# Kernel optimization log

Hardware: AMD Instinct MI355X
Metric: run time of the kernel (lower is better)

The kernel has to match this reference:

```python
import jax, jax.numpy as jnp
import numpy as np

WEIGHT = 1.0  # init kwarg: loss weight
N = 4096
D_FEAT = 128


def _pairwise_dist(x):
    # x: [n, d] -> D: [n, n] Euclidean distances (safe sqrt for grad at 0)
    sq = jnp.sum(x * x, axis=-1)
    d2 = sq[:, None] + sq[None, :] - 2.0 * (x @ x.T)
    d2 = jnp.maximum(d2, 0.0)
    pos = d2 > 1e-12
    return jnp.where(pos, jnp.sqrt(jnp.where(pos, d2, 1.0)), 0.0)


def _prim_mst(D):
    # Vectorized Prim: returns (parents, children) of the n-1 MST edges.
    # filtration value (VR complex truncated at max_dimension=1).
    n = D.shape[0]
    INF = jnp.finfo(D.dtype).max
    visited0 = jnp.zeros(n, dtype=bool).at[0].set(True)
    mind0 = D[0]
    parent0 = jnp.zeros(n, dtype=jnp.int32)

    def step(carry, _):
        visited, mind, parent = carry
        j = jnp.argmin(jnp.where(visited, INF, mind))
        pj = parent[j]
        visited = visited.at[j].set(True)
        better = (D[j] < mind) & (~visited)
        mind = jnp.where(better, D[j], mind)
        parent = jnp.where(better, j, parent)
        return (visited, mind, parent), (pj, j.astype(jnp.int32))

    _, (pjs, js) = jax.lax.scan(step, (visited0, mind0, parent0), None, length=n - 1)
    return pjs, js


def _h1_persistence(x):
    # H1 diagram for VR complex with max_dimension=1: a 1-cycle is born when a
    # non-MST edge appears; with no 2-simplices it never dies, so deaths are
    # capped at the maximal filtration value. Persistence = cap - birth.
    n = x.shape[0]
    D = _pairwise_dist(x)
    pjs, js = _prim_mst(D)
    tree = jnp.zeros((n, n), dtype=bool)
    tree = tree.at[pjs, js].set(True)
    tree = tree | tree.T
    iu = np.triu_indices(n, 1)  # static indices
    births = D[iu]              # [n*(n-1)/2]
    is_tree = tree[iu]
    cap = jnp.max(D)
    # tree edges are H0 (not H1): give them zero persistence (diagonal points)
    return jnp.where(is_tree, 0.0, cap - births)


def _wasserstein_1d(p1, p2):
    # 1-Wasserstein between equal-size persistence multisets via sorted matching
    # (deaths share a common cap per diagram, so matching by sorted persistence).
    return jnp.sum(jnp.abs(jnp.sort(p1) - jnp.sort(p2)))


def setup_inputs() -> dict:
    key = jax.random.key(0)
    k1, k2, k3, k4 = jax.random.split(key, 4)
    return {
        "graph1_features": jax.random.normal(k1, (N, D_FEAT), dtype=jnp.float32),
        "graph1_edges": jax.random.randint(k2, (2, 8 * N), 0, N, dtype=jnp.int64),
        "graph2_features": jax.random.normal(k3, (N, D_FEAT), dtype=jnp.float32),
        "graph2_edges": jax.random.randint(k4, (2, 8 * N), 0, N, dtype=jnp.int64),
    }


def reference(graph1_features, graph1_edges, graph2_features, graph2_edges):
    # edge tensors are unused: the torch forward builds VR complexes from the
    # point clouds only (build_from_points), matching the original module.
    p1 = _h1_persistence(graph1_features)
    p2 = _h1_persistence(graph2_features)
    return WEIGHT * _wasserstein_1d(p1, p2)
```

## Files before the change

### kernel.cpp

```cpp
#include <hip/hip_runtime.h>
#include <stdint.h>

#define NN 4096
#define DF 128
#define NBINS 16384
#define NSLAB 256
#define BORUVKA_ROUNDS 12

typedef __attribute__((ext_vector_type(8))) short short8;
typedef __attribute__((ext_vector_type(4))) float floatx4;
typedef __attribute__((ext_vector_type(4))) unsigned short ushort4_t;
typedef __attribute__((ext_vector_type(8))) unsigned short ushort8_t;
typedef __attribute__((ext_vector_type(4))) int int4_t;
typedef __attribute__((ext_vector_type(2))) unsigned uvec2;
typedef __attribute__((ext_vector_type(2))) int ivec2;

__device__ __forceinline__ unsigned bin_of(float v, float scale) {
  if (v < 0.f) v = 0.f;
  unsigned b = (unsigned)(v * scale);
  return b >= (unsigned)NBINS ? (unsigned)(NBINS - 1) : b;
}

__device__ __forceinline__ void gload16(const unsigned short* g, unsigned short* l) {
  __builtin_amdgcn_global_load_lds(
      (const __attribute__((address_space(1))) void*)g,
      (__attribute__((address_space(3))) void*)l, 16, 0, 0);
}

__global__ void k_rownorm(const float* __restrict__ x1, const float* __restrict__ x2,
                          float* __restrict__ sq) {
  int i = blockIdx.x * blockDim.x + threadIdx.x;
  if (i >= 2 * NN) return;
  const float* x = (i < NN) ? x1 : x2;
  int r = i & (NN - 1);
  const float* row = x + (size_t)r * DF;
  float s = 0.f;
  for (int k = 0; k < DF; ++k) s += row[k] * row[k];
  sq[i] = s;
}

__global__ __launch_bounds__(256) void k_bound(const float* __restrict__ sq,
                                               float* __restrict__ hdrf) {
  int t = threadIdx.x;
  float m = 0.f;
  for (int i = t; i < 2 * NN; i += 256) m = fmaxf(m, sq[i]);
  for (int off = 32; off > 0; off >>= 1) m = fmaxf(m, __shfl_down(m, off, 64));
  __shared__ float wm[4];
  if ((t & 63) == 0) wm[t >> 6] = m;
  __syncthreads();
  if (t == 0) {
    float mm = fmaxf(fmaxf(wm[0], wm[1]), fmaxf(wm[2], wm[3]));
    float dbound = 2.f * sqrtf(mm);
    hdrf[2] = 65535.f / dbound;
    hdrf[3] = dbound / 65535.f;
  }
}

__global__ void k_split(const float* __restrict__ x1, const float* __restrict__ x2,
                        unsigned short* __restrict__ xh, unsigned short* __restrict__ xl) {
  int i = blockIdx.x * blockDim.x + threadIdx.x;
  if (i >= 2 * NN * DF) return;
  const float* x = (i < NN * DF) ? x1 : x2;
  float v = x[i & (NN * DF - 1)];
  unsigned u = __float_as_uint(v);
  unsigned hu = u & 0xffff0000u;
  float hf = __uint_as_float(hu);
  float lf = v - hf;
  unsigned lu = __float_as_uint(lf) & 0xffff0000u;
  xh[i] = (unsigned short)(hu >> 16);
  xl[i] = (unsigned short)(lu >> 16);
}

__global__ void k_binit(int* __restrict__ comp, unsigned long long* __restrict__ compbest,
                        int* __restrict__ mstcnt, int* __restrict__ ncomp) {
  int i = blockIdx.x * blockDim.x + threadIdx.x;
  if (i >= 2 * NN) return;
  comp[i] = i & (NN - 1);
  compbest[i] = ~0ull;
  if ((i & (NN - 1)) == 0) {
    mstcnt[i >> 12] = 0;
    ncomp[i >> 12] = NN;
  }
}

#define SJ 136
__global__ __launch_bounds__(256) void k_dist(const unsigned short* __restrict__ Xhi,
                                              const unsigned short* __restrict__ Xlo,
                                              const float* __restrict__ sq,
                                              const float* __restrict__ hdrf,
                                              unsigned short* __restrict__ Qbase,
                                              unsigned* __restrict__ segmin_base,
                                              unsigned* __restrict__ caps) {
  int bi = blockIdx.y, bj = blockIdx.x;
  if (bi > bj) return;
  bool offdiag = (bi != bj);
  int g = blockIdx.z;
  const unsigned short* xh = Xhi + (size_t)g * NN * DF;
  const unsigned short* xl = Xlo + (size_t)g * NN * DF;
  const float* sqg = sq + g * NN;
  unsigned short* Q = Qbase + (size_t)g * NN * NN;
  unsigned* smg = segmin_base + (size_t)g * NN * 32;
  float qs = hdrf[2];
  int t = threadIdx.x;
  int w = t >> 6, lane = t & 63;
  int m = lane & 15, quad = lane >> 4;
  int iw = (w >> 1) * 64, jw = (w & 1) * 64;
  int i0 = bi * 128 + iw;
  int j0 = bj * 128 + jw;

  __shared__ __align__(16) unsigned short SB[128 * SJ];

  int baseRow = (w < 2) ? bi * 128 : bj * 128;
  const unsigned short* src = (w == 0 || w == 2) ? xh : xl;
  unsigned short* ldsPiece = &SB[w * 4096];
  int rsub = lane >> 2;
  int kpart = (lane & 3) ^ ((lane >> 3) & 3);
  int fr = (quad ^ ((m >> 1) & 3)) << 3;

  floatx4 acc[4][4];
#pragma unroll
  for (int ti = 0; ti < 4; ++ti)
#pragma unroll
    for (int tj = 0; tj < 4; ++tj) acc[ti][tj] = (floatx4){0.f, 0.f, 0.f, 0.f};

  for (int s = 0; s < 4; ++s) {
    int kc = s * 32;
    if (s) __syncthreads();
#pragma unroll
    for (int i = 0; i < 8; ++i) {
      const unsigned short* gp =
          src + (size_t)(baseRow + i * 16 + rsub) * DF + kc + kpart * 8;
      gload16(gp, &ldsPiece[i * 512]);
    }
    __syncthreads();
    short8 ah[4], al[4], bh[4], bl[4];
#pragma unroll
    for (int ti = 0; ti < 4; ++ti) {
      int ra = (iw + ti * 16 + m) * 32 + fr;
      int rb = (jw + ti * 16 + m) * 32 + fr;
      ah[ti] = *(const short8*)&SB[ra];
      al[ti] = *(const short8*)&SB[4096 + ra];
      bh[ti] = *(const short8*)&SB[8192 + rb];
      bl[ti] = *(const short8*)&SB[12288 + rb];
    }
#pragma unroll
    for (int ti = 0; ti < 4; ++ti)
#pragma unroll
      for (int tj = 0; tj < 4; ++tj) {
        acc[ti][tj] = __builtin_amdgcn_mfma_f32_16x16x32_bf16(ah[ti], bh[tj], acc[ti][tj], 0, 0, 0);
        acc[ti][tj] = __builtin_amdgcn_mfma_f32_16x16x32_bf16(ah[ti], bl[tj], acc[ti][tj], 0, 0, 0);
        acc[ti][tj] = __builtin_amdgcn_mfma_f32_16x16x32_bf16(al[ti], bh[tj], acc[ti][tj], 0, 0, 0);
      }
  }

  float sqj[4];
#pragma unroll
  for (int tj = 0; tj < 4; ++tj) sqj[tj] = sqg[j0 + tj * 16 + m];
  float mx = 0.f;
  ushort4_t qv[4][4];
#pragma unroll
  for (int ti = 0; ti < 4; ++ti) {
    int ib = i0 + ti * 16 + quad * 4;
    float sqiv[4];
#pragma unroll
    for (int r = 0; r < 4; ++r) sqiv[r] = sqg[ib + r];
#pragma unroll
    for (int tj = 0; tj < 4; ++tj) {
#pragma unroll
      for (int r = 0; r < 4; ++r) {
        float d2 = sqiv[r] + sqj[tj] - 2.f * acc[ti][tj][r];
        d2 = fmaxf(d2, 0.f);
        float d = (d2 > 1e-12f) ? sqrtf(d2) : 0.f;
        mx = fmaxf(mx, d);
        unsigned q = (unsigned)(d * qs + 0.5f);
        if (q > 65535u) q = 65535u;
        qv[ti][tj][r] = (unsigned short)q;
      }
    }
  }

  __syncthreads();
  unsigned short* T = SB;
  int sub = t >> 4, l16 = t & 15;
  int l31 = lane & 31, half = lane >> 5;

  auto prefill_rows = [&](int rbase, int cbase, int segidx, bool exdiag) {
#pragma unroll 4
    for (int ii = 0; ii < 16; ++ii) {
      int rr = w * 32 + ii * 2 + half;
      uvec2 vv = *(const uvec2*)&T[rr * SJ + l31 * 4];
      int row = rbase + rr;
      unsigned qq[4] = {vv[0] & 0xffffu, vv[0] >> 16, vv[1] & 0xffffu, vv[1] >> 16};
      unsigned kmin = 0xffffffffu;
#pragma unroll
      for (int u = 0; u < 4; ++u) {
        int cl = l31 * 4 + u;
        if (!exdiag || (cbase + cl) != row) {
          unsigned key = (qq[u] << 7) | (unsigned)cl;
          if (key < kmin) kmin = key;
        }
      }
#pragma unroll
      for (int off2 = 1; off2 < 32; off2 <<= 1) {
        unsigned o = (unsigned)__shfl_xor((int)kmin, off2, 32);
        if (o < kmin) kmin = o;
      }
      if (l31 == 0) smg[(size_t)row * 32 + segidx] = kmin;
    }
  };

#pragma unroll
  for (int ti = 0; ti < 4; ++ti) {
    int il = iw + ti * 16 + quad * 4;
#pragma unroll
    for (int tj = 0; tj < 4; ++tj) {
      int jl = jw + tj * 16 + m;
      *(ushort4_t*)&T[jl * SJ + il] = qv[ti][tj];
    }
  }
  __syncthreads();
#pragma unroll
  for (int k = 0; k < 8; ++k) {
    int jl = k * 16 + sub;
    int4_t v = *(const int4_t*)&T[jl * SJ + l16 * 8];
    *(int4_t*)&Q[(size_t)(bj * 128 + jl) * NN + bi * 128 + l16 * 8] = v;
  }
  prefill_rows(bj * 128, bi * 128, bi, !offdiag);

  if (offdiag) {
    __syncthreads();
#pragma unroll
    for (int ti = 0; ti < 4; ++ti) {
      int il = iw + ti * 16 + quad * 4;
#pragma unroll
      for (int tj = 0; tj < 4; ++tj) {
        int jl = jw + tj * 16 + m;
#pragma unroll
        for (int r = 0; r < 4; ++r) T[(il + r) * SJ + jl] = qv[ti][tj][r];
      }
    }
    __syncthreads();
#pragma unroll
    for (int k = 0; k < 8; ++k) {
      int il = k * 16 + sub;
      int4_t v = *(const int4_t*)&T[il * SJ + l16 * 8];
      *(int4_t*)&Q[(size_t)(bi * 128 + il) * NN + bj * 128 + l16 * 8] = v;
    }
    prefill_rows(bi * 128, bj * 128, bj, false);
  }

  for (int off = 32; off > 0; off >>= 1) mx = fmaxf(mx, __shfl_down(mx, off, 64));
  __shared__ float wmax[4];
  if (lane == 0) wmax[w] = mx;
  __syncthreads();
  if (t == 0) {
    float mm = fmaxf(fmaxf(wmax[0], wmax[1]), fmaxf(wmax[2], wmax[3]));
    atomicMax(&caps[g], __float_as_uint(mm));
  }
}

__global__ __launch_bounds__(256) void k_minedge(const unsigned short* __restrict__ Qbase,
                                                 const unsigned* __restrict__ segmin_base,
                                                 const int* __restrict__ comp_base,
                                                 unsigned long long* __restrict__ compbest_base,
                                                 const int* __restrict__ ncomp) {
  int g = blockIdx.y;
  if (ncomp[g] == 1) return;
  int w = threadIdx.x >> 6, lane = threadIdx.x & 63;
  int v = blockIdx.x * 4 + w;
  const int* comp = comp_base + g * NN;
  unsigned long long* cbest = compbest_base + (size_t)g * NN;
  int cv = comp[v];
  const unsigned* sm = segmin_base + ((size_t)g * NN + (size_t)v) * 32;

  unsigned key28 = 0xffffffffu;
  bool incomp = false;
  if (lane < 32) {
    unsigned k23 = sm[lane];
    unsigned q = k23 >> 7, cl = k23 & 127u;
    unsigned col = (unsigned)lane * 128u + cl;
    key28 = (q << 12) | col;
    incomp = (comp[col] == cv);
  }
  unsigned a = (lane < 32 && !incomp) ? key28 : 0xffffffffu;
#pragma unroll
  for (int off = 1; off < 64; off <<= 1) {
    unsigned o = (unsigned)__shfl_xor((int)a, off, 64);
    if (o < a) a = o;
  }
  unsigned best = a;

  unsigned long long flags = __ballot(lane < 32 && incomp && key28 < best);
  if (flags) {
    const unsigned short* row = Qbase + ((size_t)g * NN + (size_t)v) * NN;
    while (flags) {
      int s = (int)(__ffsll((long long)flags) - 1);
      flags &= flags - 1;
      int j = s * 128 + (lane << 1);
      unsigned pq = *(const unsigned*)&row[j];
      ivec2 cj = *(const ivec2*)&comp[j];
      unsigned k1 = (cj[0] != cv) ? ((pq & 0xffffu) << 12) | (unsigned)j : 0xffffffffu;
      unsigned k2 = (cj[1] != cv) ? ((pq >> 16) << 12) | (unsigned)(j + 1) : 0xffffffffu;
      unsigned kk = k1 < k2 ? k1 : k2;
#pragma unroll
      for (int off = 1; off < 64; off <<= 1) {
        unsigned o = (unsigned)__shfl_xor((int)kk, off, 64);
        if (o < kk) kk = o;
      }
      if (kk < best) best = kk;
    }
  }
  if (lane == 0 && best != 0xffffffffu) {
    unsigned long long b64 = ((unsigned long long)(best >> 12) << 24) |
                             ((unsigned long long)v << 12) | (best & 0xfffu);
    atomicMin(&cbest[cv], b64);
  }
}

__global__ __launch_bounds__(1024) void k_hook(unsigned long long* __restrict__ compbest_base,
                                               int* __restrict__ comp_base,
                                               const float* __restrict__ hdrf,
                                               float* __restrict__ mstw_base,
                                               int* __restrict__ mstcnt,
                                               int* __restrict__ ncomp) {
  int g = blockIdx.x;
  if (ncomp[g] == 1) return;
  unsigned long long* cb = compbest_base + (size_t)g * NN;
  int* comp = comp_base + g * NN;
  float* mstw = mstw_base + g * (NN - 1);
  float qinv = hdrf[3];
  __shared__ int par[NN];
  __shared__ unsigned char live[NN];
  __shared__ int newcnt;
  int t = threadIdx.x;
  if (t == 0) newcnt = 0;
  for (int c = t; c < NN; c += 1024) {
    unsigned long long key = cb[c];
    bool a = (key != ~0ull);
    live[c] = a ? 1 : 0;
    int p = c;
    if (a) {
      int j = (int)(key & 0xfffull);
      p = comp[j];
    }
    par[c] = p;
  }
  __syncthreads();
  for (int c = t; c < NN; c += 1024) {
    int p = par[c];
    if (p != c && par[p] == c && c < p) par[c] = c;
  }
  __syncthreads();
  for (int c = t; c < NN; c += 1024) {
    if (live[c] && par[c] != c) {
      float w = (float)((unsigned)(cb[c] >> 24)) * qinv;
      int slot = atomicAdd(&mstcnt[g], 1);
      mstw[slot] = w;
    }
  }
  __syncthreads();
  for (;;) {
    int np[NN / 1024];
    bool ch = false;
    int k = 0;
    for (int c = t; c < NN; c += 1024, ++k) {
      int p = par[c];
      int pp = par[p];
      np[k] = pp;
      if (pp != p) ch = true;
    }
    __syncthreads();
    k = 0;
    for (int c = t; c < NN; c += 1024, ++k) par[c] = np[k];
    if (!__syncthreads_or(ch)) break;
  }
  int cnt = 0;
  for (int c = t; c < NN; c += 1024)
    if (live[c] && par[c] == c) cnt++;
  for (int off = 32; off > 0; off >>= 1) cnt += __shfl_down(cnt, off, 64);
  if ((t & 63) == 0 && cnt) atomicAdd(&newcnt, cnt);
  for (int v = t; v < NN; v += 1024) comp[v] = par[comp[v]];
  for (int c = t; c < NN; c += 1024) cb[c] = ~0ull;
  __syncthreads();
  if (t == 0) ncomp[g] = newcnt;
}

__global__ __launch_bounds__(256) void k_hist(const unsigned short* __restrict__ Qbase,
                                              const unsigned* __restrict__ caps,
                                              const float* __restrict__ hdrf,
                                              unsigned* __restrict__ Hs) {
  __shared__ unsigned h[NBINS];
  int t = threadIdx.x;
  for (int i = t; i < NBINS; i += 256) h[i] = 0;
  int b = blockIdx.x;
  int g = b >> 8, s = b & (NSLAB - 1);
  const unsigned short* Q = Qbase + (size_t)g * NN * NN;
  float cap = __uint_as_float(caps[g]);
  float capmax = fmaxf(__uint_as_float(caps[0]), __uint_as_float(caps[1]));
  float scale = (float)NBINS / capmax;
  float qinv = hdrf[3];
  __syncthreads();
  for (int p = s; p < NN / 2; p += NSLAB) {
#pragma unroll
    for (int half = 0; half < 2; ++half) {
      int rrow = half ? (NN - 1 - p) : p;
      const unsigned short* row = Q + (size_t)rrow * NN;
      int j0 = rrow + 1;
      int ja = (j0 + 7) & ~7;
      if (t < ja - j0)
        atomicAdd(&h[bin_of(cap - (float)row[j0 + t] * qinv, scale)], 1u);
      int nch = (NN - ja) >> 3;
      for (int c = t; c < nch; c += 256) {
        ushort8_t v8 = *(const ushort8_t*)&row[ja + c * 8];
#pragma unroll
        for (int u = 0; u < 8; ++u)
          atomicAdd(&h[bin_of(cap - (float)v8[u] * qinv, scale)], 1u);
      }
    }
  }
  __syncthreads();
  unsigned* slab = Hs + (size_t)b * NBINS;
  for (int i = t; i < NBINS; i += 256) slab[i] = h[i];
}

__global__ void k_treefix(const float* __restrict__ twbase, const unsigned* __restrict__ caps,
                          unsigned* __restrict__ Hs) {
  int g = blockIdx.y;
  unsigned* hist = Hs + (size_t)(g * NSLAB) * NBINS;
  float cap = __uint_as_float(caps[g]);
  float capmax = fmaxf(__uint_as_float(caps[0]), __uint_as_float(caps[1]));
  float scale = (float)NBINS / capmax;
  int idx = blockIdx.x * blockDim.x + threadIdx.x;
  if (idx < NN - 1) {
    float w = twbase[g * (NN - 1) + idx];
    atomicSub(&hist[bin_of(cap - w, scale)], 1u);
    atomicAdd(&hist[0], 1u);
  }
}

__global__ __launch_bounds__(256) void k_merge(const unsigned* __restrict__ Hs,
                                               unsigned* __restrict__ Hm) {
  int id = blockIdx.x * 256 + threadIdx.x;
  int g = id >> 14;
  int i = id & (NBINS - 1);
  const unsigned* base = Hs + (size_t)(g * NSLAB) * NBINS + i;
  unsigned sum = 0;
  for (int s = 0; s < NSLAB; ++s) sum += base[(size_t)s * NBINS];
  Hm[id] = sum;
}

__global__ __launch_bounds__(256) void k_w1(const unsigned* __restrict__ Hm,
                                            const unsigned* __restrict__ caps,
                                            float* __restrict__ out) {
  int t = threadIdx.x;
  const int PB = NBINS / 256;
  int base = t * PB;
  long long tsum = 0;
  for (int i = 0; i < PB; ++i)
    tsum += (long long)(int)(Hm[base + i] - Hm[NBINS + base + i]);
  int lane = t & 63, wid = t >> 6;
  long long incl = tsum;
  for (int off = 1; off < 64; off <<= 1) {
    long long o = __shfl_up(incl, off, 64);
    if (lane >= off) incl += o;
  }
  __shared__ long long wtot[4];
  if (lane == 63) wtot[wid] = incl;
  __syncthreads();
  long long run = incl - tsum;
  for (int w = 0; w < wid; ++w) run += wtot[w];
  unsigned long long local = 0;
  for (int i = 0; i < PB; ++i) {
    run += (long long)(int)(Hm[base + i] - Hm[NBINS + base + i]);
    local += (unsigned long long)(run < 0 ? -run : run);
  }
  for (int off = 32; off > 0; off >>= 1) local += __shfl_down(local, off, 64);
  __shared__ unsigned long long wl[4];
  if (lane == 0) wl[wid] = local;
  __syncthreads();
  if (t == 0) {
    float capmax = fmaxf(__uint_as_float(caps[0]), __uint_as_float(caps[1]));
    double dt = (double)capmax / (double)NBINS;
    out[0] = (float)((double)(wl[0] + wl[1] + wl[2] + wl[3]) * dt);
  }
}

__global__ void k_fail(float* out) { out[0] = -1234567.0f; }

extern "C" void kernel_launch(void* const* d_in, const int* in_sizes, int n_in,
                              void* d_out, int out_size, void* d_ws, size_t ws_size,
                              hipStream_t stream) {
  const float* x1 = (const float*)d_in[0];
  const float* x2 = (const float*)d_in[2];
  float* out = (float*)d_out;
  char* ws = (char*)d_ws;

  const size_t offQ = 0;
  const size_t offS = 2ull * NN * NN * 2ull;
  const size_t offHm = offS + 2ull * NSLAB * NBINS * 4ull;
  const size_t offHdr = offHm + 2ull * NBINS * 4ull;
  const size_t offSq = offHdr + 64;
  const size_t offTw = offSq + 2ull * NN * 4ull;
  const size_t offCb = (offTw + 2ull * (NN - 1) * 4ull + 7ull) & ~7ull;
  const size_t offSeg = offCb + 2ull * NN * 8ull;
  const size_t offCp = offSeg + 2ull * NN * 32ull * 4ull;
  const size_t offMeta = offCp + 2ull * NN * 4ull;
  const size_t needed = offMeta + 64;
  if (ws_size < needed) {
    hipLaunchKernelGGL(k_fail, dim3(1), dim3(1), 0, stream, out);
    return;
  }

  unsigned short* Qbase = (unsigned short*)(ws + offQ);
  unsigned* Hs = (unsigned*)(ws + offS);
  unsigned short* Xhi = (unsigned short*)(ws + offS);
  unsigned short* Xlo = (unsigned short*)(ws + offS + 2ull * NN * DF * 2ull);
  unsigned* Hm = (unsigned*)(ws + offHm);
  unsigned* caps = (unsigned*)(ws + offHdr);
  float* hdrf = (float*)(ws + offHdr);
  float* sq = (float*)(ws + offSq);
  float* tw = (float*)(ws + offTw);
  unsigned long long* compbest = (unsigned long long*)(ws + offCb);
  unsigned* segmin = (unsigned*)(ws + offSeg);
  int* comp = (int*)(ws + offCp);
  int* mstcnt = (int*)(ws + offMeta);
  int* ncomp = (int*)(ws + offMeta + 8);

  hipMemsetAsync(ws + offHdr, 0, 64, stream);

  hipLaunchKernelGGL(k_rownorm, dim3((2 * NN + 255) / 256), dim3(256), 0, stream, x1, x2, sq);
  hipLaunchKernelGGL(k_bound, dim3(1), dim3(256), 0, stream, sq, hdrf);
  hipLaunchKernelGGL(k_split, dim3((2 * NN * DF + 255) / 256), dim3(256), 0, stream,
                     x1, x2, Xhi, Xlo);
  hipLaunchKernelGGL(k_binit, dim3((2 * NN + 255) / 256), dim3(256), 0, stream,
                     comp, compbest, mstcnt, ncomp);
  hipLaunchKernelGGL(k_dist, dim3(NN / 128, NN / 128, 2), dim3(256), 0, stream,
                     Xhi, Xlo, sq, hdrf, Qbase, segmin, caps);
  for (int r = 0; r < BORUVKA_ROUNDS; ++r) {
    hipLaunchKernelGGL(k_minedge, dim3(NN / 4, 2), dim3(256), 0, stream,
                       Qbase, segmin, comp, compbest, ncomp);
    hipLaunchKernelGGL(k_hook, dim3(2), dim3(1024), 0, stream,
                       compbest, comp, hdrf, tw, mstcnt, ncomp);
  }
  hipLaunchKernelGGL(k_hist, dim3(2 * NSLAB), dim3(256), 0, stream, Qbase, caps, hdrf, Hs);
  hipLaunchKernelGGL(k_treefix, dim3(16, 2), dim3(256), 0, stream, tw, caps, Hs);
  hipLaunchKernelGGL(k_merge, dim3(2 * NBINS / 256), dim3(256), 0, stream, Hs, Hm);
  hipLaunchKernelGGL(k_w1, dim3(1), dim3(256), 0, stream, Hm, caps, out);
}
```

Baseline: 349.5 us.

## Fuse Boruvka min-edge and hook kernels with last-block-done pattern

Merges the per-round min-edge search and the component hooking step into one kernel. The last block to finish, detected through an atomic counter per graph, performs the hooking and pointer-jumping. This halves the number of launches across the Boruvka rounds. Blocks grow to 1024 threads with a 20KB shared-memory footprint. That may lower occupancy for the min-edge part and puts the serial hook step at the tail of the grid.

```diff
diff --git a/kernel.cpp b/kernel.cpp
--- a/kernel.cpp
+++ b/kernel.cpp
@@ -72,14 +72,17 @@
 }
 
 __global__ void k_binit(int* __restrict__ comp, unsigned long long* __restrict__ compbest,
-                        int* __restrict__ mstcnt, int* __restrict__ ncomp) {
+                        int* __restrict__ mstcnt, int* __restrict__ ncomp,
+                        int* __restrict__ done) {
   int i = blockIdx.x * blockDim.x + threadIdx.x;
   if (i >= 2 * NN) return;
   comp[i] = i & (NN - 1);
   compbest[i] = ~0ull;
   if ((i & (NN - 1)) == 0) {
-    mstcnt[i >> 12] = 0;
-    ncomp[i >> 12] = NN;
+    int g = i >> 12;
+    mstcnt[g] = 0;
+    ncomp[g] = NN;
+    done[g] = 0;
   }
 }
 
@@ -259,90 +262,92 @@
   }
 }
 
-__global__ __launch_bounds__(256) void k_minedge(const unsigned short* __restrict__ Qbase,
-                                                 const unsigned* __restrict__ segmin_base,
-                                                 const int* __restrict__ comp_base,
-                                                 unsigned long long* __restrict__ compbest_base,
-                                                 const int* __restrict__ ncomp) {
+__global__ __launch_bounds__(1024) void k_round(
+    const unsigned short* __restrict__ Qbase,
+    const unsigned* __restrict__ segmin_base,
+    int* __restrict__ comp_base,
+    unsigned long long* __restrict__ compbest_base,
+    const float* __restrict__ hdrf,
+    float* __restrict__ mstw_base,
+    int* __restrict__ mstcnt,
+    int* __restrict__ ncomp,
+    int* __restrict__ done) {
   int g = blockIdx.y;
   if (ncomp[g] == 1) return;
-  int w = threadIdx.x >> 6, lane = threadIdx.x & 63;
-  int v = blockIdx.x * 4 + w;
-  const int* comp = comp_base + g * NN;
+  int t = threadIdx.x;
+  int w = t >> 6, lane = t & 63;
+  int v = blockIdx.x * 16 + w;
+  int* comp = comp_base + g * NN;
   unsigned long long* cbest = compbest_base + (size_t)g * NN;
-  int cv = comp[v];
-  const unsigned* sm = segmin_base + ((size_t)g * NN + (size_t)v) * 32;
-
-  unsigned key28 = 0xffffffffu;
-  bool incomp = false;
-  if (lane < 32) {
-    unsigned k23 = sm[lane];
-    unsigned q = k23 >> 7, cl = k23 & 127u;
-    unsigned col = (unsigned)lane * 128u + cl;
-    key28 = (q << 12) | col;
-    incomp = (comp[col] == cv);
-  }
-  unsigned a = (lane < 32 && !incomp) ? key28 : 0xffffffffu;
-#pragma unroll
-  for (int off = 1; off < 64; off <<= 1) {
-    unsigned o = (unsigned)__shfl_xor((int)a, off, 64);
-    if (o < a) a = o;
-  }
-  unsigned best = a;
-
-  unsigned long long flags = __ballot(lane < 32 && incomp && key28 < best);
-  if (flags) {
-    const unsigned short* row = Qbase + ((size_t)g * NN + (size_t)v) * NN;
-    while (flags) {
-      int s = (int)(__ffsll((long long)flags) - 1);
-      flags &= flags - 1;
-      int j = s * 128 + (lane << 1);
-      unsigned pq = *(const unsigned*)&row[j];
-      ivec2 cj = *(const ivec2*)&comp[j];
-      unsigned k1 = (cj[0] != cv) ? ((pq & 0xffffu) << 12) | (unsigned)j : 0xffffffffu;
-      unsigned k2 = (cj[1] != cv) ? ((pq >> 16) << 12) | (unsigned)(j + 1) : 0xffffffffu;
-      unsigned kk = k1 < k2 ? k1 : k2;
-#pragma unroll
-      for (int off = 1; off < 64; off <<= 1) {
-        unsigned o = (unsigned)__shfl_xor((int)kk, off, 64);
-        if (o < kk) kk = o;
-      }
-      if (kk < best) best = kk;
-    }
-  }
-  if (lane == 0 && best != 0xffffffffu) {
-    unsigned long long b64 = ((unsigned long long)(best >> 12) << 24) |
-                             ((unsigned long long)v << 12) | (best & 0xfffu);
-    atomicMin(&cbest[cv], b64);
-  }
-}
-
-__global__ __launch_bounds__(1024) void k_hook(unsigned long long* __restrict__ compbest_base,
-                                               int* __restrict__ comp_base,
-                                               const float* __restrict__ hdrf,
-                                               float* __restrict__ mstw_base,
-                                               int* __restrict__ mstcnt,
-                                               int* __restrict__ ncomp) {
-  int g = blockIdx.x;
-  if (ncomp[g] == 1) return;
-  unsigned long long* cb = compbest_base + (size_t)g * NN;
-  int* comp = comp_base + g * NN;
+
+  {
+    int cv = comp[v];
+    const unsigned* sm = segmin_base + ((size_t)g * NN + (size_t)v) * 32;
+    unsigned key28 = 0xffffffffu;
+    bool incomp = false;
+    if (lane < 32) {
+      unsigned k23 = sm[lane];
+      unsigned q = k23 >> 7, cl = k23 & 127u;
+      unsigned col = (unsigned)lane * 128u + cl;
+      key28 = (q << 12) | col;
+      incomp = (comp[col] == cv);
+    }
+    unsigned a = (lane < 32 && !incomp) ? key28 : 0xffffffffu;
+#pragma unroll
+    for (int off = 1; off < 64; off <<= 1) {
+      unsigned o = (unsigned)__shfl_xor((int)a, off, 64);
+      if (o < a) a = o;
+    }
+    unsigned best = a;
+
+    unsigned long long flags = __ballot(lane < 32 && incomp && key28 < best);
+    if (flags) {
+      const unsigned short* row = Qbase + ((size_t)g * NN + (size_t)v) * NN;
+      while (flags) {
+        int s = (int)(__ffsll((long long)flags) - 1);
+        flags &= flags - 1;
+        int j = s * 128 + (lane << 1);
+        unsigned pq = *(const unsigned*)&row[j];
+        ivec2 cj = *(const ivec2*)&comp[j];
+        unsigned k1 = (cj[0] != cv) ? ((pq & 0xffffu) << 12) | (unsigned)j : 0xffffffffu;
+        unsigned k2 = (cj[1] != cv) ? ((pq >> 16) << 12) | (unsigned)(j + 1) : 0xffffffffu;
+        unsigned kk = k1 < k2 ? k1 : k2;
+#pragma unroll
+        for (int off = 1; off < 64; off <<= 1) {
+          unsigned o = (unsigned)__shfl_xor((int)kk, off, 64);
+          if (o < kk) kk = o;
+        }
+        if (kk < best) best = kk;
+      }
+    }
+    if (lane == 0 && best != 0xffffffffu) {
+      unsigned long long b64 = ((unsigned long long)(best >> 12) << 24) |
+                               ((unsigned long long)v << 12) | (best & 0xfffu);
+      atomicMin(&cbest[cv], b64);
+    }
+  }
+
+  __threadfence();
+  __syncthreads();
+  __shared__ int amlast;
+  if (t == 0) amlast = (atomicAdd(&done[g], 1) == (int)gridDim.x - 1) ? 1 : 0;
+  __syncthreads();
+  if (!amlast) return;
+
+  float qinv = hdrf[3];
+  unsigned long long* cb = cbest;
   float* mstw = mstw_base + g * (NN - 1);
-  float qinv = hdrf[3];
   __shared__ int par[NN];
   __shared__ unsigned char live[NN];
   __shared__ int newcnt;
-  int t = threadIdx.x;
   if (t == 0) newcnt = 0;
   for (int c = t; c < NN; c += 1024) {
-    unsigned long long key = cb[c];
+    unsigned long long key =
+        __hip_atomic_load(&cb[c], __ATOMIC_RELAXED, __HIP_MEMORY_SCOPE_AGENT);
     bool a = (key != ~0ull);
     live[c] = a ? 1 : 0;
     int p = c;
-    if (a) {
-      int j = (int)(key & 0xfffull);
-      p = comp[j];
-    }
+    if (a) p = comp[(int)(key & 0xfffull)];
     par[c] = p;
   }
   __syncthreads();
@@ -353,9 +358,11 @@
   __syncthreads();
   for (int c = t; c < NN; c += 1024) {
     if (live[c] && par[c] != c) {
-      float w = (float)((unsigned)(cb[c] >> 24)) * qinv;
+      unsigned long long key =
+          __hip_atomic_load(&cb[c], __ATOMIC_RELAXED, __HIP_MEMORY_SCOPE_AGENT);
+      float wgt = (float)((unsigned)(key >> 24)) * qinv;
       int slot = atomicAdd(&mstcnt[g], 1);
-      mstw[slot] = w;
+      mstw[slot] = wgt;
     }
   }
   __syncthreads();
@@ -379,10 +386,13 @@
     if (live[c] && par[c] == c) cnt++;
   for (int off = 32; off > 0; off >>= 1) cnt += __shfl_down(cnt, off, 64);
   if ((t & 63) == 0 && cnt) atomicAdd(&newcnt, cnt);
-  for (int v = t; v < NN; v += 1024) comp[v] = par[comp[v]];
+  for (int u = t; u < NN; u += 1024) comp[u] = par[comp[u]];
   for (int c = t; c < NN; c += 1024) cb[c] = ~0ull;
   __syncthreads();
-  if (t == 0) ncomp[g] = newcnt;
+  if (t == 0) {
+    ncomp[g] = newcnt;
+    done[g] = 0;
+  }
 }
 
 __global__ __launch_bounds__(256) void k_hist(const unsigned short* __restrict__ Qbase,
@@ -525,6 +535,7 @@
   int* comp = (int*)(ws + offCp);
   int* mstcnt = (int*)(ws + offMeta);
   int* ncomp = (int*)(ws + offMeta + 8);
+  int* done = (int*)(ws + offMeta + 16);
 
   hipMemsetAsync(ws + offHdr, 0, 64, stream);
 
@@ -533,14 +544,12 @@
   hipLaunchKernelGGL(k_split, dim3((2 * NN * DF + 255) / 256), dim3(256), 0, stream,
                      x1, x2, Xhi, Xlo);
   hipLaunchKernelGGL(k_binit, dim3((2 * NN + 255) / 256), dim3(256), 0, stream,
-                     comp, compbest, mstcnt, ncomp);
+                     comp, compbest, mstcnt, ncomp, done);
   hipLaunchKernelGGL(k_dist, dim3(NN / 128, NN / 128, 2), dim3(256), 0, stream,
                      Xhi, Xlo, sq, hdrf, Qbase, segmin, caps);
   for (int r = 0; r < BORUVKA_ROUNDS; ++r) {
-    hipLaunchKernelGGL(k_minedge, dim3(NN / 4, 2), dim3(256), 0, stream,
-                       Qbase, segmin, comp, compbest, ncomp);
-    hipLaunchKernelGGL(k_hook, dim3(2), dim3(1024), 0, stream,
-                       compbest, comp, hdrf, tw, mstcnt, ncomp);
+    hipLaunchKernelGGL(k_round, dim3(NN / 16, 2), dim3(1024), 0, stream,
+                       Qbase, segmin, comp, compbest, hdrf, tw, mstcnt, ncomp, done);
   }
   hipLaunchKernelGGL(k_hist, dim3(2 * NSLAB), dim3(256), 0, stream, Qbase, caps, hdrf, Hs);
   hipLaunchKernelGGL(k_treefix, dim3(16, 2), dim3(256), 0, stream, tw, caps, Hs);
```

Result: slower. 708.2 us (+102.7%).

## Move per-row segment-min computation from distance kernel into histogram pass

Applied to the files above, without the earlier changes.

The per-row 128-column segment minima used by the Boruvka min-edge search are no longer computed in the distance kernel. The histogram kernel, which now runs before the Boruvka rounds, computes them while it reads Q. The histogram pass now reads full rows rather than only the upper triangle. This is meant to lighten the distance kernel's epilogue and reuse the Q read the histogram pass already does, at the cost of roughly doubling the histogram kernel's global reads.

```diff
diff --git a/kernel.cpp b/kernel.cpp
--- a/kernel.cpp
+++ b/kernel.cpp
@@ -12,7 +12,6 @@
 typedef __attribute__((ext_vector_type(4))) unsigned short ushort4_t;
 typedef __attribute__((ext_vector_type(8))) unsigned short ushort8_t;
 typedef __attribute__((ext_vector_type(4))) int int4_t;
-typedef __attribute__((ext_vector_type(2))) unsigned uvec2;
 typedef __attribute__((ext_vector_type(2))) int ivec2;
 
 __device__ __forceinline__ unsigned bin_of(float v, float scale) {
@@ -89,7 +88,6 @@
                                               const float* __restrict__ sq,
                                               const float* __restrict__ hdrf,
                                               unsigned short* __restrict__ Qbase,
-                                              unsigned* __restrict__ segmin_base,
                                               unsigned* __restrict__ caps) {
   int bi = blockIdx.y, bj = blockIdx.x;
   if (bi > bj) return;
@@ -99,7 +97,6 @@
   const unsigned short* xl = Xlo + (size_t)g * NN * DF;
   const float* sqg = sq + g * NN;
   unsigned short* Q = Qbase + (size_t)g * NN * NN;
-  unsigned* smg = segmin_base + (size_t)g * NN * 32;
   float qs = hdrf[2];
   int t = threadIdx.x;
   int w = t >> 6, lane = t & 63;
@@ -182,32 +179,6 @@
   __syncthreads();
   unsigned short* T = SB;
   int sub = t >> 4, l16 = t & 15;
-  int l31 = lane & 31, half = lane >> 5;
-
-  auto prefill_rows = [&](int rbase, int cbase, int segidx, bool exdiag) {
-#pragma unroll 4
-    for (int ii = 0; ii < 16; ++ii) {
-      int rr = w * 32 + ii * 2 + half;
-      uvec2 vv = *(const uvec2*)&T[rr * SJ + l31 * 4];
-      int row = rbase + rr;
-      unsigned qq[4] = {vv[0] & 0xffffu, vv[0] >> 16, vv[1] & 0xffffu, vv[1] >> 16};
-      unsigned kmin = 0xffffffffu;
-#pragma unroll
-      for (int u = 0; u < 4; ++u) {
-        int cl = l31 * 4 + u;
-        if (!exdiag || (cbase + cl) != row) {
-          unsigned key = (qq[u] << 7) | (unsigned)cl;
-          if (key < kmin) kmin = key;
-        }
-      }
-#pragma unroll
-      for (int off2 = 1; off2 < 32; off2 <<= 1) {
-        unsigned o = (unsigned)__shfl_xor((int)kmin, off2, 32);
-        if (o < kmin) kmin = o;
-      }
-      if (l31 == 0) smg[(size_t)row * 32 + segidx] = kmin;
-    }
-  };
 
 #pragma unroll
   for (int ti = 0; ti < 4; ++ti) {
@@ -225,7 +196,6 @@
     int4_t v = *(const int4_t*)&T[jl * SJ + l16 * 8];
     *(int4_t*)&Q[(size_t)(bj * 128 + jl) * NN + bi * 128 + l16 * 8] = v;
   }
-  prefill_rows(bj * 128, bi * 128, bi, !offdiag);
 
   if (offdiag) {
     __syncthreads();
@@ -246,7 +216,6 @@
       int4_t v = *(const int4_t*)&T[il * SJ + l16 * 8];
       *(int4_t*)&Q[(size_t)(bi * 128 + il) * NN + bj * 128 + l16 * 8] = v;
     }
-    prefill_rows(bi * 128, bj * 128, bj, false);
   }
 
   for (int off = 32; off > 0; off >>= 1) mx = fmaxf(mx, __shfl_down(mx, off, 64));
@@ -257,6 +226,57 @@
     float mm = fmaxf(fmaxf(wmax[0], wmax[1]), fmaxf(wmax[2], wmax[3]));
     atomicMax(&caps[g], __float_as_uint(mm));
   }
+}
+
+__global__ __launch_bounds__(256) void k_hist(const unsigned short* __restrict__ Qbase,
+                                              const unsigned* __restrict__ caps,
+                                              const float* __restrict__ hdrf,
+                                              unsigned* __restrict__ Hs,
+                                              unsigned* __restrict__ segmin_base) {
+  __shared__ unsigned h[NBINS];
+  int t = threadIdx.x;
+  for (int i = t; i < NBINS; i += 256) h[i] = 0;
+  int b = blockIdx.x;
+  int g = b >> 8, s = b & (NSLAB - 1);
+  const unsigned short* Q = Qbase + (size_t)g * NN * NN;
+  unsigned* smg = segmin_base + (size_t)g * NN * 32;
+  float cap = __uint_as_float(caps[g]);
+  float capmax = fmaxf(__uint_as_float(caps[0]), __uint_as_float(caps[1]));
+  float scale = (float)NBINS / capmax;
+  float qinv = hdrf[3];
+  int w = t >> 6, lane = t & 63;
+  __syncthreads();
+  for (int k = 0; k < 16; ++k) {
+    int row = s + k * NSLAB;
+    const unsigned short* rp = Q + (size_t)row * NN;
+#pragma unroll
+    for (int pp = 0; pp < 2; ++pp) {
+      int c = pp * 256 + w * 64 + lane;
+      int col0 = c * 8;
+      ushort8_t v8 = *(const ushort8_t*)&rp[col0];
+      unsigned kmin = 0xffffffffu;
+#pragma unroll
+      for (int u = 0; u < 8; ++u) {
+        int col = col0 + u;
+        unsigned q = (unsigned short)v8[u];
+        if (col > row)
+          atomicAdd(&h[bin_of(cap - (float)q * qinv, scale)], 1u);
+        if (col != row) {
+          unsigned key = (q << 7) | (unsigned)(col & 127);
+          if (key < kmin) kmin = key;
+        }
+      }
+#pragma unroll
+      for (int off = 1; off < 16; off <<= 1) {
+        unsigned o = (unsigned)__shfl_xor((int)kmin, off, 16);
+        if (o < kmin) kmin = o;
+      }
+      if ((lane & 15) == 0) smg[(size_t)row * 32 + (c >> 4)] = kmin;
+    }
+  }
+  __syncthreads();
+  unsigned* slab = Hs + (size_t)b * NBINS;
+  for (int i = t; i < NBINS; i += 256) slab[i] = h[i];
 }
 
 __global__ __launch_bounds__(256) void k_minedge(const unsigned short* __restrict__ Qbase,
@@ -385,44 +405,6 @@
   if (t == 0) ncomp[g] = newcnt;
 }
 
-__global__ __launch_bounds__(256) void k_hist(const unsigned short* __restrict__ Qbase,
-                                              const unsigned* __restrict__ caps,
-                                              const float* __restrict__ hdrf,
-                                              unsigned* __restrict__ Hs) {
-  __shared__ unsigned h[NBINS];
-  int t = threadIdx.x;
-  for (int i = t; i < NBINS; i += 256) h[i] = 0;
-  int b = blockIdx.x;
-  int g = b >> 8, s = b & (NSLAB - 1);
-  const unsigned short* Q = Qbase + (size_t)g * NN * NN;
-  float cap = __uint_as_float(caps[g]);
-  float capmax = fmaxf(__uint_as_float(caps[0]), __uint_as_float(caps[1]));
-  float scale = (float)NBINS / capmax;
-  float qinv = hdrf[3];
-  __syncthreads();
-  for (int p = s; p < NN / 2; p += NSLAB) {
-#pragma unroll
-    for (int half = 0; half < 2; ++half) {
-      int rrow = half ? (NN - 1 - p) : p;
-      const unsigned short* row = Q + (size_t)rrow * NN;
-      int j0 = rrow + 1;
-      int ja = (j0 + 7) & ~7;
-      if (t < ja - j0)
-        atomicAdd(&h[bin_of(cap - (float)row[j0 + t] * qinv, scale)], 1u);
-      int nch = (NN - ja) >> 3;
-      for (int c = t; c < nch; c += 256) {
-        ushort8_t v8 = *(const ushort8_t*)&row[ja + c * 8];
-#pragma unroll
-        for (int u = 0; u < 8; ++u)
-          atomicAdd(&h[bin_of(cap - (float)v8[u] * qinv, scale)], 1u);
-      }
-    }
-  }
-  __syncthreads();
-  unsigned* slab = Hs + (size_t)b * NBINS;
-  for (int i = t; i < NBINS; i += 256) slab[i] = h[i];
-}
-
 __global__ void k_treefix(const float* __restrict__ twbase, const unsigned* __restrict__ caps,
                           unsigned* __restrict__ Hs) {
   int g = blockIdx.y;
@@ -535,14 +517,15 @@
   hipLaunchKernelGGL(k_binit, dim3((2 * NN + 255) / 256), dim3(256), 0, stream,
                      comp, compbest, mstcnt, ncomp);
   hipLaunchKernelGGL(k_dist, dim3(NN / 128, NN / 128, 2), dim3(256), 0, stream,
-                     Xhi, Xlo, sq, hdrf, Qbase, segmin, caps);
+                     Xhi, Xlo, sq, hdrf, Qbase, caps);
+  hipLaunchKernelGGL(k_hist, dim3(2 * NSLAB), dim3(256), 0, stream,
+                     Qbase, caps, hdrf, Hs, segmin);
   for (int r = 0; r < BORUVKA_ROUNDS; ++r) {
     hipLaunchKernelGGL(k_minedge, dim3(NN / 4, 2), dim3(256), 0, stream,
                        Qbase, segmin, comp, compbest, ncomp);
     hipLaunchKernelGGL(k_hook, dim3(2), dim3(1024), 0, stream,
                        compbest, comp, hdrf, tw, mstcnt, ncomp);
   }
-  hipLaunchKernelGGL(k_hist, dim3(2 * NSLAB), dim3(256), 0, stream, Qbase, caps, hdrf, Hs);
   hipLaunchKernelGGL(k_treefix, dim3(16, 2), dim3(256), 0, stream, tw, caps, Hs);
   hipLaunchKernelGGL(k_merge, dim3(2 * NBINS / 256), dim3(256), 0, stream, Hs, Hm);
   hipLaunchKernelGGL(k_w1, dim3(1), dim3(256), 0, stream, Hm, caps, out);
```

New measurement: 338.9 us. -3.0%, faster.
